# Optimization experiments

Measured on AMD Instinct MI355X. Metric: run time of the kernel, lower is better.

## Reference

```python
import jax, jax.numpy as jnp
import numpy as np

B, S, E = 2, 2048, 1024
H, W_SIZE = 16, 128
D = E // H


def setup_inputs() -> dict:
    key = jax.random.key(0)
    ks = jax.random.split(key, 7)
    std = 1.0 / np.sqrt(E)
    return {
        "x": jax.random.normal(ks[0], (B, S, E), dtype=jnp.float32),
        "Wq": jax.random.normal(ks[1], (E, E), dtype=jnp.float32) * std,
        "bq": jax.random.normal(ks[2], (E,), dtype=jnp.float32) * std,
        "Wk": jax.random.normal(ks[3], (E, E), dtype=jnp.float32) * std,
        "bk": jax.random.normal(ks[4], (E,), dtype=jnp.float32) * std,
        "Wv": jax.random.normal(ks[5], (E, E), dtype=jnp.float32) * std,
        "bv": jax.random.normal(ks[6], (E,), dtype=jnp.float32) * std,
    }


def reference(x, Wq, bq, Wk, bk, Wv, bv):
    b, s, e = x.shape
    scale = jnp.float32(D) ** -0.5
    # torch Linear: y = x @ W.T + b
    # Faithful to original: view() splits [b, s, e] -> [b, H, s, D] WITHOUT transpose
    q = (x @ Wq.T + bq).reshape(b, H, s, D)
    k = (x @ Wk.T + bk).reshape(b, H, s, D)
    v = (x @ Wv.T + bv).reshape(b, H, s, D)
    # window: scores kept for j in [max(0, i - w), min(s, i + w)), zeros elsewhere
    i = jnp.arange(s)[:, None]
    j = jnp.arange(s)[None, :]
    mask = (j >= i - W_SIZE) & (j < i + W_SIZE)  # [s, s]
    qk = jnp.einsum("bhid,bhjd->bhij", q, k)
    # out-of-window entries are ZERO (not -inf) and softmax is over the full row,
    # exactly matching the original zero-padded score tensor.
    scores = jnp.where(mask, qk, 0.0) * scale
    probs = jax.nn.softmax(scores, axis=-1)
    out = jnp.einsum("bhij,bhjd->bhid", probs, v)  # [b, H, s, D]
    out = out.transpose(0, 2, 1, 3).reshape(b, s, e)
    return out
```

## Files before the change

kernel.cpp:

```cpp
#include <hip/hip_runtime.h>
#include <math.h>

#define S_LEN 2048
#define E_DIM 1024
#define NHEAD 16
#define HD 64
#define WIN 128
#define NB 2
#define MTOT (NB * S_LEN)
#define NMAT 3072

typedef float f32x4 __attribute__((ext_vector_type(4)));
typedef short bf16x8 __attribute__((ext_vector_type(8)));

#define GLOAD_LDS(g, l) __builtin_amdgcn_global_load_lds( \
    (const __attribute__((address_space(1))) unsigned int*)(g), \
    (__attribute__((address_space(3))) unsigned int*)(l), 16, 0, 0)

__device__ __forceinline__ unsigned short f2bf(float f) {
    unsigned u = __float_as_uint(f);
    u += 0x7fffu + ((u >> 16) & 1u);
    return (unsigned short)(u >> 16);
}
__device__ __forceinline__ float bf2f(unsigned short u) {
    return __uint_as_float(((unsigned)u) << 16);
}

__global__ __launch_bounds__(256) void convert_kernel(
    const float* __restrict__ x, const float* __restrict__ wq,
    const float* __restrict__ wk, const float* __restrict__ wv,
    unsigned short* __restrict__ xb, unsigned short* __restrict__ wb)
{
    const int NXQ = MTOT * E_DIM / 4;
    const int NWQ = E_DIM * E_DIM / 4;
    const int TOT = NXQ + 3 * NWQ;
    for (int i = blockIdx.x * 256 + threadIdx.x; i < TOT; i += gridDim.x * 256) {
        const float* src; unsigned short* dst; int off;
        if (i < NXQ)               { src = x;  dst = xb;                     off = i; }
        else if (i < NXQ + NWQ)    { src = wq; dst = wb;                     off = i - NXQ; }
        else if (i < NXQ + 2*NWQ)  { src = wk; dst = wb + E_DIM * E_DIM;     off = i - NXQ - NWQ; }
        else                       { src = wv; dst = wb + 2 * E_DIM * E_DIM; off = i - NXQ - 2*NWQ; }
        float4 v = ((const float4*)src)[off];
        ushort4 o;
        o.x = f2bf(v.x); o.y = f2bf(v.y); o.z = f2bf(v.z); o.w = f2bf(v.w);
        ((ushort4*)dst)[off] = o;
    }
}

__global__ __launch_bounds__(256) void gemm_mfma(
    const unsigned short* __restrict__ Ab, const unsigned short* __restrict__ Bb,
    const float* __restrict__ bq, const float* __restrict__ bk, const float* __restrict__ bv,
    unsigned short* __restrict__ Qb, unsigned short* __restrict__ Kb,
    unsigned short* __restrict__ Vb)
{
    __shared__ __align__(256) unsigned short As[128 * 64];
    __shared__ __align__(256) unsigned short Bs[128 * 64];
    const int tid  = threadIdx.x;
    const int lane = tid & 63;
    const int w    = tid >> 6;
    const int wm   = w & 1, wn = w >> 1;
    const int m0   = blockIdx.y * 128;
    const int n0   = blockIdx.x * 128;
    const int l15  = lane & 15, l4 = lane >> 4;

    f32x4 acc[16] = {};

    for (int k0 = 0; k0 < E_DIM; k0 += 64) {
        #pragma unroll
        for (int is = 0; is < 4; ++is) {
            int gid = is * 256 + tid;
            int r = gid >> 3, sl = gid & 7;
            int gran = sl ^ (r & 7);
            int wbs = is * 256 + (tid & 192);
            GLOAD_LDS(Ab + (size_t)(m0 + r) * E_DIM + k0 + gran * 8, As + wbs * 8);
            GLOAD_LDS(Bb + (size_t)(n0 + r) * E_DIM + k0 + gran * 8, Bs + wbs * 8);
        }
        __syncthreads();
        #pragma unroll
        for (int kk = 0; kk < 2; ++kk) {
            bf16x8 af[4], bfr[4];
            int sa = (kk * 4 + l4) ^ (l15 & 7);
            #pragma unroll
            for (int t = 0; t < 4; ++t) {
                int ra = wm * 64 + t * 16 + l15;
                af[t]  = *(const bf16x8*)&As[ra * 64 + sa * 8];
                int rb = wn * 64 + t * 16 + l15;
                bfr[t] = *(const bf16x8*)&Bs[rb * 64 + sa * 8];
            }
            #pragma unroll
            for (int mt = 0; mt < 4; ++mt)
                #pragma unroll
                for (int nt = 0; nt < 4; ++nt)
                    acc[mt * 4 + nt] = __builtin_amdgcn_mfma_f32_16x16x32_bf16(
                        af[mt], bfr[nt], acc[mt * 4 + nt], 0, 0, 0);
        }
        __syncthreads();
    }

    const int sel = n0 >> 10;
    const float* bias = (sel == 0) ? bq : ((sel == 1) ? bk : bv);
    unsigned short* Yb = (sel == 0) ? Qb : ((sel == 1) ? Kb : Vb);
    const int nbase = (n0 & 1023) + wn * 64;
    #pragma unroll
    for (int mt = 0; mt < 4; ++mt) {
        #pragma unroll
        for (int nt = 0; nt < 4; ++nt) {
            int n = nbase + nt * 16 + l15;
            int c = n >> 6, d = n & 63;
            float bb = bias[n];
            #pragma unroll
            for (int r = 0; r < 4; ++r) {
                int m = m0 + wm * 64 + mt * 16 + l4 * 4 + r;
                int b = m >> 11, s = m & 2047;
                int h = s >> 7;
                int i = ((s & 127) << 4) + c;
                Yb[(((size_t)(b * 16 + h) * S_LEN + i) << 6) + d] =
                    f2bf(acc[mt * 4 + nt][r] + bb);
            }
        }
    }
}

__global__ __launch_bounds__(256) void transpose_v(
    const unsigned short* __restrict__ Vb, unsigned short* __restrict__ VTb)
{
    __shared__ unsigned short t[64][72];
    const int bh = blockIdx.y;
    const int it0 = blockIdx.x * 64;
    const int tid = threadIdx.x;
    const unsigned short* src = Vb + ((size_t)bh * S_LEN + it0) * HD;
    {
        int r = tid >> 2, c0 = (tid & 3) * 16;
        #pragma unroll
        for (int k = 0; k < 4; ++k) {
            ushort4 a = *(const ushort4*)&src[r * 64 + c0 + k * 4];
            *(ushort4*)&t[r][c0 + k * 4] = a;
        }
    }
    __syncthreads();
    {
        int d = tid >> 2, seg = (tid & 3) * 16;
        unsigned short v[16];
        #pragma unroll
        for (int k = 0; k < 16; ++k) v[k] = t[seg + k][d];
        unsigned short* dst = VTb + ((size_t)bh * HD + d) * S_LEN + it0 + seg;
        #pragma unroll
        for (int k = 0; k < 4; ++k)
            *(ushort4*)&dst[k * 4] = *(const ushort4*)&v[k * 4];
    }
}

__global__ __launch_bounds__(256) void vtot_kernel(const unsigned short* __restrict__ VTb,
                                                   float* __restrict__ vt)
{
    int bh = blockIdx.x;
    int d = threadIdx.x >> 2, part = threadIdx.x & 3;
    const unsigned short* p = VTb + ((size_t)bh * HD + d) * S_LEN + part * 512;
    float s = 0.f;
    for (int it = 0; it < 128; ++it) {
        ushort4 a = ((const ushort4*)p)[it];
        s += bf2f(a.x) + bf2f(a.y) + bf2f(a.z) + bf2f(a.w);
    }
    __shared__ float red[64][4];
    red[d][part] = s;
    __syncthreads();
    if (part == 0) vt[bh * HD + d] = red[d][0] + red[d][1] + red[d][2] + red[d][3];
}

__global__ __launch_bounds__(256) void attn_mfma(
    const unsigned short* __restrict__ Qb, const unsigned short* __restrict__ Kb,
    const unsigned short* __restrict__ VTb, const float* __restrict__ vtot,
    float* __restrict__ out)
{
    __shared__ __align__(256) unsigned short qs[64 * 64];
    __shared__ __align__(256) unsigned short ks[2][64 * 64];
    __shared__ __align__(256) unsigned short vts[2][64 * 64];
    __shared__ __align__(16)  unsigned short ps[4][16 * 72];

    const int qt = blockIdx.x, bh = blockIdx.y;
    const int b = bh >> 4, h = bh & 15;
    const int i0 = qt * 64;
    const int tid = threadIdx.x;
    const int w = tid >> 6, lane = tid & 63;
    const int l15 = lane & 15, quad = lane >> 4;

    const unsigned short* Qp = Qb + (size_t)bh * S_LEN * HD;
    const unsigned short* Kp = Kb + (size_t)bh * S_LEN * HD;
    const unsigned short* Vp = VTb + (size_t)bh * HD * S_LEN;

    #pragma unroll
    for (int it = 0; it < 2; ++it) {
        int gid = it * 256 + tid;
        int r = gid >> 3, sl = gid & 7;
        int gran = sl ^ (r & 7);
        int wbs = it * 256 + (tid & 192);
        GLOAD_LDS(Qp + (size_t)(i0 + r) * HD + gran * 8, qs + wbs * 8);
    }
    {
        const int jc0 = i0 - WIN;
        #pragma unroll
        for (int it = 0; it < 2; ++it) {
            int gid = it * 256 + tid;
            int r = gid >> 3, sl = gid & 7;
            int gran = sl ^ (r & 7);
            int wbs = it * 256 + (tid & 192);
            int jg = jc0 + r; jg = jg < 0 ? 0 : (jg > S_LEN - 1 ? S_LEN - 1 : jg);
            GLOAD_LDS(Kp + (size_t)jg * HD + gran * 8, ks[0] + wbs * 8);
            int jc = jc0 + gran * 8; jc = jc < 0 ? 0 : (jc > S_LEN - 8 ? S_LEN - 8 : jc);
            GLOAD_LDS(Vp + (size_t)r * S_LEN + jc, vts[0] + wbs * 8);
        }
    }
    __syncthreads();

    bf16x8 aq[2];
    {
        int row = w * 16 + l15;
        aq[0] = *(const bf16x8*)&qs[(row * 8 + (quad ^ (row & 7))) * 8];
        aq[1] = *(const bf16x8*)&qs[(row * 8 + ((4 + quad) ^ (row & 7))) * 8];
    }
    int jlo4[4], jhi4[4];
    #pragma unroll
    for (int reg = 0; reg < 4; ++reg) {
        int i = i0 + w * 16 + quad * 4 + reg;
        jlo4[reg] = (i - WIN > 0) ? i - WIN : 0;
        jhi4[reg] = (i + WIN < S_LEN) ? i + WIN : S_LEN;
    }
    bf16x8 bones;
    #pragma unroll
    for (int t = 0; t < 8; ++t) bones[t] = (short)0x3F80;

    f32x4 acc_o[4] = {};
    f32x4 acc_sum = {};
    unsigned short* psw = &ps[w][0];

    for (int c = 0; c < 5; ++c) {
        const int cb = c & 1;
        const int jc0 = i0 - WIN + c * 64;

        if (c < 4) {
            const int jn0 = jc0 + 64;
            #pragma unroll
            for (int it = 0; it < 2; ++it) {
                int gid = it * 256 + tid;
                int r = gid >> 3, sl = gid & 7;
                int gran = sl ^ (r & 7);
                int wbs = it * 256 + (tid & 192);
                int jg = jn0 + r; jg = jg < 0 ? 0 : (jg > S_LEN - 1 ? S_LEN - 1 : jg);
                GLOAD_LDS(Kp + (size_t)jg * HD + gran * 8, ks[1 - cb] + wbs * 8);
                int jc = jn0 + gran * 8; jc = jc < 0 ? 0 : (jc > S_LEN - 8 ? S_LEN - 8 : jc);
                GLOAD_LDS(Vp + (size_t)r * S_LEN + jc, vts[1 - cb] + wbs * 8);
            }
        }

        f32x4 sacc[4] = {};
        const unsigned short* kb = ks[cb];
        #pragma unroll
        for (int kk = 0; kk < 2; ++kk) {
            #pragma unroll
            for (int jt = 0; jt < 4; ++jt) {
                int row = jt * 16 + l15;
                bf16x8 bk = *(const bf16x8*)&kb[(row * 8 + ((kk * 4 + quad) ^ (row & 7))) * 8];
                sacc[jt] = __builtin_amdgcn_mfma_f32_16x16x32_bf16(aq[kk], bk, sacc[jt], 0, 0, 0);
            }
        }

        #pragma unroll
        for (int jt = 0; jt < 4; ++jt) {
            int jg = jc0 + jt * 16 + l15;
            #pragma unroll
            for (int reg = 0; reg < 4; ++reg) {
                bool valid = (jg >= jlo4[reg]) && (jg < jhi4[reg]);
                float p = valid ? __expf(sacc[jt][reg] * 0.125f) - 1.f : 0.f;
                psw[(quad * 4 + reg) * 72 + jt * 16 + l15] = f2bf(p);
            }
        }
        bf16x8 ap0 = *(const bf16x8*)&psw[l15 * 72 + quad * 8];
        bf16x8 ap1 = *(const bf16x8*)&psw[l15 * 72 + 32 + quad * 8];

        const unsigned short* vb = vts[cb];
        #pragma unroll
        for (int kst = 0; kst < 2; ++kst) {
            bf16x8 ap = kst ? ap1 : ap0;
            #pragma unroll
            for (int dt = 0; dt < 4; ++dt) {
                int row = dt * 16 + l15;
                bf16x8 bv_ = *(const bf16x8*)&vb[(row * 8 + ((kst * 4 + quad) ^ (row & 7))) * 8];
                acc_o[dt] = __builtin_amdgcn_mfma_f32_16x16x32_bf16(ap, bv_, acc_o[dt], 0, 0, 0);
            }
            acc_sum = __builtin_amdgcn_mfma_f32_16x16x32_bf16(ap, bones, acc_sum, 0, 0, 0);
        }
        __syncthreads();
    }

    const float* vtp = vtot + bh * HD;
    float vtv[4];
    #pragma unroll
    for (int dt = 0; dt < 4; ++dt) vtv[dt] = vtp[dt * 16 + l15];
    #pragma unroll
    for (int reg = 0; reg < 4; ++reg) {
        int i = i0 + w * 16 + quad * 4 + reg;
        float inv = 1.f / (acc_sum[reg] + (float)S_LEN);
        float* op = out + (((size_t)(b * S_LEN + i)) * NHEAD + h) * HD;
        #pragma unroll
        for (int dt = 0; dt < 4; ++dt)
            op[dt * 16 + l15] = (acc_o[dt][reg] + vtv[dt]) * inv;
    }
}

extern "C" void kernel_launch(void* const* d_in, const int* in_sizes, int n_in,
                              void* d_out, int out_size, void* d_ws, size_t ws_size,
                              hipStream_t stream)
{
    const float* x  = (const float*)d_in[0];
    const float* Wq = (const float*)d_in[1];
    const float* bq = (const float*)d_in[2];
    const float* Wk = (const float*)d_in[3];
    const float* bk = (const float*)d_in[4];
    const float* Wv = (const float*)d_in[5];
    const float* bv = (const float*)d_in[6];
    float* out = (float*)d_out;

    const size_t NY = (size_t)MTOT * E_DIM;
    unsigned short* xb  = (unsigned short*)d_ws;
    unsigned short* wb  = xb + NY;
    unsigned short* Qb  = wb + (size_t)3 * E_DIM * E_DIM;
    unsigned short* Kb  = Qb + NY;
    unsigned short* Vb  = Kb + NY;
    float* vt = (float*)(Vb + NY);
    unsigned short* VTb = xb;

    convert_kernel<<<1792, 256, 0, stream>>>(x, Wq, Wk, Wv, xb, wb);
    gemm_mfma<<<dim3(NMAT / 128, MTOT / 128), 256, 0, stream>>>(xb, wb, bq, bk, bv, Qb, Kb, Vb);
    transpose_v<<<dim3(S_LEN / 64, NB * NHEAD), 256, 0, stream>>>(Vb, VTb);
    vtot_kernel<<<NB * NHEAD, 256, 0, stream>>>(VTb, vt);
    attn_mfma<<<dim3(S_LEN / 64, NB * NHEAD), 256, 0, stream>>>(Qb, Kb, VTb, vt, out);
}
```

Measured before the change: 160.6 us.

## Fuse V column-sum into transpose and double attention query tile to 128

The per-column V sum is now computed inside the transpose kernel with shuffle reductions and atomicAdd into a memset-zeroed buffer, which removes the separate vtot kernel. The attention kernel now processes 128 queries per block, with each wave handling two 16-row query tiles. Each loaded K/V chunk therefore serves twice the queries, and the chunk range is clamped to valid keys so edge blocks no longer load padded chunks. In exchange there are more registers and LDS per block, half as many blocks, an extra memset launch, and atomics whose ordering makes the V sums nondeterministic.

Result: faster. 152.6 us (-5.0%).

```diff
diff --git a/kernel.cpp b/kernel.cpp
--- a/kernel.cpp
+++ b/kernel.cpp
@@ -121,8 +121,9 @@
     }
 }
 
-__global__ __launch_bounds__(256) void transpose_v(
-    const unsigned short* __restrict__ Vb, unsigned short* __restrict__ VTb)
+__global__ __launch_bounds__(256) void transpose_vtot(
+    const unsigned short* __restrict__ Vb, unsigned short* __restrict__ VTb,
+    float* __restrict__ vt)
 {
     __shared__ unsigned short t[64][72];
     const int bh = blockIdx.y;
@@ -141,30 +142,17 @@
     {
         int d = tid >> 2, seg = (tid & 3) * 16;
         unsigned short v[16];
-        #pragma unroll
-        for (int k = 0; k < 16; ++k) v[k] = t[seg + k][d];
+        float s = 0.f;
+        #pragma unroll
+        for (int k = 0; k < 16; ++k) { v[k] = t[seg + k][d]; s += bf2f(v[k]); }
         unsigned short* dst = VTb + ((size_t)bh * HD + d) * S_LEN + it0 + seg;
         #pragma unroll
         for (int k = 0; k < 4; ++k)
             *(ushort4*)&dst[k * 4] = *(const ushort4*)&v[k * 4];
-    }
-}
-
-__global__ __launch_bounds__(256) void vtot_kernel(const unsigned short* __restrict__ VTb,
-                                                   float* __restrict__ vt)
-{
-    int bh = blockIdx.x;
-    int d = threadIdx.x >> 2, part = threadIdx.x & 3;
-    const unsigned short* p = VTb + ((size_t)bh * HD + d) * S_LEN + part * 512;
-    float s = 0.f;
-    for (int it = 0; it < 128; ++it) {
-        ushort4 a = ((const ushort4*)p)[it];
-        s += bf2f(a.x) + bf2f(a.y) + bf2f(a.z) + bf2f(a.w);
-    }
-    __shared__ float red[64][4];
-    red[d][part] = s;
-    __syncthreads();
-    if (part == 0) vt[bh * HD + d] = red[d][0] + red[d][1] + red[d][2] + red[d][3];
+        s += __shfl_xor(s, 1);
+        s += __shfl_xor(s, 2);
+        if ((tid & 3) == 0) atomicAdd(&vt[bh * HD + d], s);
+    }
 }
 
 __global__ __launch_bounds__(256) void attn_mfma(
@@ -172,14 +160,14 @@
     const unsigned short* __restrict__ VTb, const float* __restrict__ vtot,
     float* __restrict__ out)
 {
-    __shared__ __align__(256) unsigned short qs[64 * 64];
+    __shared__ __align__(256) unsigned short qs[128 * 64];
     __shared__ __align__(256) unsigned short ks[2][64 * 64];
     __shared__ __align__(256) unsigned short vts[2][64 * 64];
-    __shared__ __align__(16)  unsigned short ps[4][16 * 72];
+    __shared__ __align__(16)  unsigned short ps[4][32 * 72];
 
     const int qt = blockIdx.x, bh = blockIdx.y;
     const int b = bh >> 4, h = bh & 15;
-    const int i0 = qt * 64;
+    const int i0 = qt * 128;
     const int tid = threadIdx.x;
     const int w = tid >> 6, lane = tid & 63;
     const int l15 = lane & 15, quad = lane >> 4;
@@ -187,6 +175,19 @@
     const unsigned short* Qp = Qb + (size_t)bh * S_LEN * HD;
     const unsigned short* Kp = Kb + (size_t)bh * S_LEN * HD;
     const unsigned short* Vp = VTb + (size_t)bh * HD * S_LEN;
+
+    #pragma unroll
+    for (int it = 0; it < 4; ++it) {
+        int gid = it * 256 + tid;
+        int r = gid >> 3, sl = gid & 7;
+        int gran = sl ^ (r & 7);
+        int wbs = it * 256 + (tid & 192);
+        GLOAD_LDS(Qp + (size_t)(i0 + r) * HD + gran * 8, qs + wbs * 8);
+    }
+
+    const int j_begin = (i0 - WIN > 0) ? i0 - WIN : 0;
+    const int j_end   = (i0 + 256 < S_LEN) ? i0 + 256 : S_LEN;
+    const int n_ch    = (j_end - j_begin) >> 6;
 
     #pragma unroll
     for (int it = 0; it < 2; ++it) {
@@ -194,50 +195,31 @@
         int r = gid >> 3, sl = gid & 7;
         int gran = sl ^ (r & 7);
         int wbs = it * 256 + (tid & 192);
-        GLOAD_LDS(Qp + (size_t)(i0 + r) * HD + gran * 8, qs + wbs * 8);
-    }
-    {
-        const int jc0 = i0 - WIN;
-        #pragma unroll
-        for (int it = 0; it < 2; ++it) {
-            int gid = it * 256 + tid;
-            int r = gid >> 3, sl = gid & 7;
-            int gran = sl ^ (r & 7);
-            int wbs = it * 256 + (tid & 192);
-            int jg = jc0 + r; jg = jg < 0 ? 0 : (jg > S_LEN - 1 ? S_LEN - 1 : jg);
-            GLOAD_LDS(Kp + (size_t)jg * HD + gran * 8, ks[0] + wbs * 8);
-            int jc = jc0 + gran * 8; jc = jc < 0 ? 0 : (jc > S_LEN - 8 ? S_LEN - 8 : jc);
-            GLOAD_LDS(Vp + (size_t)r * S_LEN + jc, vts[0] + wbs * 8);
-        }
+        GLOAD_LDS(Kp + (size_t)(j_begin + r) * HD + gran * 8, ks[0] + wbs * 8);
+        GLOAD_LDS(Vp + (size_t)r * S_LEN + j_begin + gran * 8, vts[0] + wbs * 8);
     }
     __syncthreads();
 
-    bf16x8 aq[2];
-    {
-        int row = w * 16 + l15;
-        aq[0] = *(const bf16x8*)&qs[(row * 8 + (quad ^ (row & 7))) * 8];
-        aq[1] = *(const bf16x8*)&qs[(row * 8 + ((4 + quad) ^ (row & 7))) * 8];
-    }
-    int jlo4[4], jhi4[4];
-    #pragma unroll
-    for (int reg = 0; reg < 4; ++reg) {
-        int i = i0 + w * 16 + quad * 4 + reg;
-        jlo4[reg] = (i - WIN > 0) ? i - WIN : 0;
-        jhi4[reg] = (i + WIN < S_LEN) ? i + WIN : S_LEN;
+    bf16x8 aq[2][2];
+    #pragma unroll
+    for (int q2 = 0; q2 < 2; ++q2) {
+        int row = w * 32 + q2 * 16 + l15;
+        aq[q2][0] = *(const bf16x8*)&qs[(row * 8 + (quad ^ (row & 7))) * 8];
+        aq[q2][1] = *(const bf16x8*)&qs[(row * 8 + ((4 + quad) ^ (row & 7))) * 8];
     }
     bf16x8 bones;
     #pragma unroll
     for (int t = 0; t < 8; ++t) bones[t] = (short)0x3F80;
 
-    f32x4 acc_o[4] = {};
-    f32x4 acc_sum = {};
+    f32x4 acc_o[2][4] = {};
+    f32x4 acc_sum[2] = {};
     unsigned short* psw = &ps[w][0];
 
-    for (int c = 0; c < 5; ++c) {
+    for (int c = 0; c < n_ch; ++c) {
         const int cb = c & 1;
-        const int jc0 = i0 - WIN + c * 64;
-
-        if (c < 4) {
+        const int jc0 = j_begin + c * 64;
+
+        if (c + 1 < n_ch) {
             const int jn0 = jc0 + 64;
             #pragma unroll
             for (int it = 0; it < 2; ++it) {
@@ -245,14 +227,12 @@
                 int r = gid >> 3, sl = gid & 7;
                 int gran = sl ^ (r & 7);
                 int wbs = it * 256 + (tid & 192);
-                int jg = jn0 + r; jg = jg < 0 ? 0 : (jg > S_LEN - 1 ? S_LEN - 1 : jg);
-                GLOAD_LDS(Kp + (size_t)jg * HD + gran * 8, ks[1 - cb] + wbs * 8);
-                int jc = jn0 + gran * 8; jc = jc < 0 ? 0 : (jc > S_LEN - 8 ? S_LEN - 8 : jc);
-                GLOAD_LDS(Vp + (size_t)r * S_LEN + jc, vts[1 - cb] + wbs * 8);
-            }
-        }
-
-        f32x4 sacc[4] = {};
+                GLOAD_LDS(Kp + (size_t)(jn0 + r) * HD + gran * 8, ks[1 - cb] + wbs * 8);
+                GLOAD_LDS(Vp + (size_t)r * S_LEN + jn0 + gran * 8, vts[1 - cb] + wbs * 8);
+            }
+        }
+
+        f32x4 sacc[2][4] = {};
         const unsigned short* kb = ks[cb];
         #pragma unroll
         for (int kk = 0; kk < 2; ++kk) {
@@ -260,34 +240,44 @@
             for (int jt = 0; jt < 4; ++jt) {
                 int row = jt * 16 + l15;
                 bf16x8 bk = *(const bf16x8*)&kb[(row * 8 + ((kk * 4 + quad) ^ (row & 7))) * 8];
-                sacc[jt] = __builtin_amdgcn_mfma_f32_16x16x32_bf16(aq[kk], bk, sacc[jt], 0, 0, 0);
-            }
-        }
-
-        #pragma unroll
-        for (int jt = 0; jt < 4; ++jt) {
-            int jg = jc0 + jt * 16 + l15;
-            #pragma unroll
-            for (int reg = 0; reg < 4; ++reg) {
-                bool valid = (jg >= jlo4[reg]) && (jg < jhi4[reg]);
-                float p = valid ? __expf(sacc[jt][reg] * 0.125f) - 1.f : 0.f;
-                psw[(quad * 4 + reg) * 72 + jt * 16 + l15] = f2bf(p);
-            }
-        }
-        bf16x8 ap0 = *(const bf16x8*)&psw[l15 * 72 + quad * 8];
-        bf16x8 ap1 = *(const bf16x8*)&psw[l15 * 72 + 32 + quad * 8];
+                sacc[0][jt] = __builtin_amdgcn_mfma_f32_16x16x32_bf16(aq[0][kk], bk, sacc[0][jt], 0, 0, 0);
+                sacc[1][jt] = __builtin_amdgcn_mfma_f32_16x16x32_bf16(aq[1][kk], bk, sacc[1][jt], 0, 0, 0);
+            }
+        }
+
+        #pragma unroll
+        for (int q2 = 0; q2 < 2; ++q2) {
+            #pragma unroll
+            for (int jt = 0; jt < 4; ++jt) {
+                int jg = jc0 + jt * 16 + l15;
+                #pragma unroll
+                for (int reg = 0; reg < 4; ++reg) {
+                    int i = i0 + w * 32 + q2 * 16 + quad * 4 + reg;
+                    bool valid = (jg >= i - WIN) && (jg < i + WIN);
+                    float p = valid ? __expf(sacc[q2][jt][reg] * 0.125f) - 1.f : 0.f;
+                    psw[(q2 * 16 + quad * 4 + reg) * 72 + jt * 16 + l15] = f2bf(p);
+                }
+            }
+        }
+        bf16x8 ap[2][2];
+        #pragma unroll
+        for (int q2 = 0; q2 < 2; ++q2) {
+            ap[q2][0] = *(const bf16x8*)&psw[(q2 * 16 + l15) * 72 + quad * 8];
+            ap[q2][1] = *(const bf16x8*)&psw[(q2 * 16 + l15) * 72 + 32 + quad * 8];
+        }
 
         const unsigned short* vb = vts[cb];
         #pragma unroll
         for (int kst = 0; kst < 2; ++kst) {
-            bf16x8 ap = kst ? ap1 : ap0;
             #pragma unroll
             for (int dt = 0; dt < 4; ++dt) {
                 int row = dt * 16 + l15;
                 bf16x8 bv_ = *(const bf16x8*)&vb[(row * 8 + ((kst * 4 + quad) ^ (row & 7))) * 8];
-                acc_o[dt] = __builtin_amdgcn_mfma_f32_16x16x32_bf16(ap, bv_, acc_o[dt], 0, 0, 0);
-            }
-            acc_sum = __builtin_amdgcn_mfma_f32_16x16x32_bf16(ap, bones, acc_sum, 0, 0, 0);
+                acc_o[0][dt] = __builtin_amdgcn_mfma_f32_16x16x32_bf16(ap[0][kst], bv_, acc_o[0][dt], 0, 0, 0);
+                acc_o[1][dt] = __builtin_amdgcn_mfma_f32_16x16x32_bf16(ap[1][kst], bv_, acc_o[1][dt], 0, 0, 0);
+            }
+            acc_sum[0] = __builtin_amdgcn_mfma_f32_16x16x32_bf16(ap[0][kst], bones, acc_sum[0], 0, 0, 0);
+            acc_sum[1] = __builtin_amdgcn_mfma_f32_16x16x32_bf16(ap[1][kst], bones, acc_sum[1], 0, 0, 0);
         }
         __syncthreads();
     }
@@ -297,13 +287,16 @@
     #pragma unroll
     for (int dt = 0; dt < 4; ++dt) vtv[dt] = vtp[dt * 16 + l15];
     #pragma unroll
-    for (int reg = 0; reg < 4; ++reg) {
-        int i = i0 + w * 16 + quad * 4 + reg;
-        float inv = 1.f / (acc_sum[reg] + (float)S_LEN);
-        float* op = out + (((size_t)(b * S_LEN + i)) * NHEAD + h) * HD;
-        #pragma unroll
-        for (int dt = 0; dt < 4; ++dt)
-            op[dt * 16 + l15] = (acc_o[dt][reg] + vtv[dt]) * inv;
+    for (int q2 = 0; q2 < 2; ++q2) {
+        #pragma unroll
+        for (int reg = 0; reg < 4; ++reg) {
+            int i = i0 + w * 32 + q2 * 16 + quad * 4 + reg;
+            float inv = 1.f / (acc_sum[q2][reg] + (float)S_LEN);
+            float* op = out + (((size_t)(b * S_LEN + i)) * NHEAD + h) * HD;
+            #pragma unroll
+            for (int dt = 0; dt < 4; ++dt)
+                op[dt * 16 + l15] = (acc_o[q2][dt][reg] + vtv[dt]) * inv;
+        }
     }
 }
 
@@ -331,7 +324,7 @@
 
     convert_kernel<<<1792, 256, 0, stream>>>(x, Wq, Wk, Wv, xb, wb);
     gemm_mfma<<<dim3(NMAT / 128, MTOT / 128), 256, 0, stream>>>(xb, wb, bq, bk, bv, Qb, Kb, Vb);
-    transpose_v<<<dim3(S_LEN / 64, NB * NHEAD), 256, 0, stream>>>(Vb, VTb);
-    vtot_kernel<<<NB * NHEAD, 256, 0, stream>>>(VTb, vt);
-    attn_mfma<<<dim3(S_LEN / 64, NB * NHEAD), 256, 0, stream>>>(Qb, Kb, VTb, vt, out);
-}
+    hipMemsetAsync(vt, 0, (size_t)NB * NHEAD * HD * sizeof(float), stream);
+    transpose_vtot<<<dim3(S_LEN / 64, NB * NHEAD), 256, 0, stream>>>(Vb, VTb, vt);
+    attn_mfma<<<dim3(S_LEN / 128, NB * NHEAD), 256, 0, stream>>>(Qb, Kb, VTb, vt, out);
+}
```
